# Performance work log

Hardware: AMD Instinct MI355X
Metric: run time of the kernel (lower is better)

## Reference

```python
import jax, jax.numpy as jnp
import numpy as np

B, IN, H, Z = 2048, 1024, 1024, 256


def setup_inputs() -> dict:
    key = jax.random.key(0)
    ks = jax.random.split(key, 17)
    s = 1.0 / np.sqrt(H)  # matches reset_parameters uniform(-stdv, stdv)
    u = lambda k, shape: jax.random.uniform(k, shape, minval=-s, maxval=s, dtype=jnp.float32)
    return {
        'src_x': jax.random.normal(ks[0], (B, IN), dtype=jnp.float32),
        'h': jax.random.normal(ks[1], (B, H), dtype=jnp.float32),
        'c': jax.random.normal(ks[2], (B, H), dtype=jnp.float32),
        'src_meta': jax.random.normal(ks[3], (B, Z), dtype=jnp.float32),
        'zh_w': u(ks[4], (4 * Z, Z)),
        'zh_b': u(ks[5], (4 * Z,)),
        'zx_w': u(ks[6], (4 * Z, Z)),
        'zx_b': u(ks[7], (4 * Z,)),
        'zb_w': u(ks[8], (4 * Z, Z)),
        'dh_w': u(ks[9], (4, H, Z)),
        'dx_w': u(ks[10], (4, H, Z)),
        'db_w': u(ks[11], (4, H, Z)),
        'db_b': u(ks[12], (4, H)),
        'w_h': u(ks[13], (4, H, H)),
        'w_x': u(ks[14], (4, H, IN)),
        'ln_w': u(ks[15], (4, H)),
        'ln_b': u(ks[16], (4, H)),
    }


def reference(src_x, h, c, src_meta, zh_w, zh_b, zx_w, zx_b, zb_w,
              dh_w, dx_w, db_w, db_b, w_h, w_x, ln_w, ln_b):
    b = src_x.shape[0]
    # hypernetwork projections, reshaped to [B, 4 gates, Z]
    zh = (src_meta @ zh_w.T + zh_b).reshape(b, 4, -1)
    zx = (src_meta @ zx_w.T + zx_b).reshape(b, 4, -1)
    zb = (src_meta @ zb_w.T).reshape(b, 4, -1)
    # per-gate scaling vectors d_h, d_x and bias d_b: [B, 4, H]
    d_h = jnp.einsum('bgz,ghz->bgh', zh, dh_w)
    d_x = jnp.einsum('bgz,ghz->bgh', zx, dx_w)
    d_b = jnp.einsum('bgz,ghz->bgh', zb, db_w) + db_b[None]
    # main LSTM matmuls: [B, 4, H]
    wh = jnp.einsum('ghj,bj->bgh', w_h, h)
    wx = jnp.einsum('ghj,bj->bgh', w_x, src_x)
    y = d_h * wh + d_x * wx + d_b
    # per-gate LayerNorm over hidden dim (eps = 1e-5, torch default)
    mu = jnp.mean(y, axis=-1, keepdims=True)
    var = jnp.var(y, axis=-1, keepdims=True)
    yn = (y - mu) * jax.lax.rsqrt(var + 1e-5) * ln_w[None] + ln_b[None]
    i, f, g, o = yn[:, 0], yn[:, 1], yn[:, 2], yn[:, 3]
    c_next = jax.nn.sigmoid(f) * c + jax.nn.sigmoid(i) * jnp.tanh(g)
    h_next = jax.nn.sigmoid(o) * jnp.tanh(c_next)
    return (h_next, c_next)
```

## Files before the change

### kernel.cpp

```cpp
#include <hip/hip_runtime.h>

typedef __attribute__((ext_vector_type(4))) float f32x4;
typedef __attribute__((ext_vector_type(16))) float f32x16;
typedef __attribute__((ext_vector_type(8))) short bf16x8;

#define DEVFN static __device__ __forceinline__

DEVFN unsigned short f2bf(float f) {
  union { float f; unsigned u; } x; x.f = f;
  unsigned r = x.u + 0x7fffu + ((x.u >> 16) & 1u);
  return (unsigned short)(r >> 16);
}
DEVFN float bf2f(unsigned short u) {
  union { unsigned u; float f; } x; x.u = ((unsigned)u) << 16;
  return x.f;
}

DEVFN void gload_lds16(const unsigned short* g, unsigned short* l) {
  __builtin_amdgcn_global_load_lds(
      (const __attribute__((address_space(1))) unsigned int*)g,
      (__attribute__((address_space(3))) unsigned int*)l, 16, 0, 0);
}

#define NSEG 8
struct SegTable {
  const float* src[NSEG];
  unsigned short* dst[NSEG];
  int chunks[NSEG];
};

__global__ __launch_bounds__(256) void prep_kernel(
    SegTable st, int castChunks,
    const float* __restrict__ zh_w, const float* __restrict__ zx_w,
    const float* __restrict__ zb_w, unsigned short* __restrict__ WzT,
    const float* __restrict__ zh_b, const float* __restrict__ zx_b,
    const float* __restrict__ db_b, const float* __restrict__ dh_w,
    const float* __restrict__ dx_w, float* __restrict__ F) {
  __shared__ float T[64][65];
  const int tid = threadIdx.x;
  int b = blockIdx.x;

  if (b < castChunks) {
    int c = b, s = 0;
    while (c >= st.chunks[s]) { c -= st.chunks[s]; ++s; }
    const float* src = st.src[s] + (long)c * 4096;
    unsigned short* dst = st.dst[s] + (long)c * 4096;
#pragma unroll
    for (int i = 0; i < 4; ++i) {
      float4 v = *(const float4*)(src + tid * 4 + i * 1024);
      ushort4 o;
      o.x = f2bf(v.x); o.y = f2bf(v.y); o.z = f2bf(v.z); o.w = f2bf(v.w);
      *(ushort4*)(dst + tid * 4 + i * 1024) = o;
    }
    return;
  }
  b -= castChunks;

  if (b < 192) {
    const int zz = b >> 4, rem = b & 15;
    const int t = zz >> 2, g = zz & 3;
    const float* src =
        (t == 0 ? zh_w : (t == 1 ? zx_w : zb_w)) + (long)g * 65536;
    unsigned short* dst = WzT + (long)zz * 65536;
    const int j0 = (rem & 3) * 64, k0 = (rem >> 2) * 64;
    const int jr = tid >> 2, kc = (tid & 3) * 16;
#pragma unroll
    for (int i = 0; i < 4; ++i) {
      float4 v = *(const float4*)(src + (long)(j0 + jr) * 256 + k0 + kc + i * 4);
      T[jr][kc + i * 4 + 0] = v.x;
      T[jr][kc + i * 4 + 1] = v.y;
      T[jr][kc + i * 4 + 2] = v.z;
      T[jr][kc + i * 4 + 3] = v.w;
    }
    __syncthreads();
    const int kr = tid >> 2, jc = (tid & 3) * 16;
    unsigned short tmp[16];
#pragma unroll
    for (int i = 0; i < 16; ++i) tmp[i] = f2bf(T[jc + i][kr]);
    *(bf16x8*)(dst + (long)(k0 + kr) * 256 + j0 + jc) = *(bf16x8*)&tmp[0];
    *(bf16x8*)(dst + (long)(k0 + kr) * 256 + j0 + jc + 8) = *(bf16x8*)&tmp[8];
    return;
  }
  b -= 192;

  if (b >= 128) {
    const int idx = (b - 128) * 1024 + tid * 4;
    *(float4*)(F + 8192 + idx) = *(const float4*)(db_b + idx);
    return;
  }
  const int wgid = b * 4 + (tid >> 6);
  const int lane = tid & 63;
  const int t = wgid >> 8, g = (wgid >> 6) & 3, hbase = (wgid & 63) * 16;
  const float* zb = (t == 0 ? zh_b : zx_b) + g * 256;
  const float* dw = (t == 0 ? dh_w : dx_w) + (long)g * 262144;
  float4 zv = *(const float4*)(zb + lane * 4);
#pragma unroll
  for (int i = 0; i < 16; ++i) {
    const int h = hbase + i;
    float4 wv = *(const float4*)(dw + (long)h * 256 + lane * 4);
    float s = zv.x * wv.x + zv.y * wv.y + zv.z * wv.z + zv.w * wv.w;
#pragma unroll
    for (int off = 32; off; off >>= 1) s += __shfl_down(s, off);
    if (lane == 0) F[(t * 4 + g) * 1024 + h] = s;
  }
}

DEVFN void gemm128_body(const unsigned short* __restrict__ A,
                        const unsigned short* __restrict__ W,
                        unsigned short* __restrict__ C,
                        const float* __restrict__ bias,
                        int lda, int ldb, int ldc, int K,
                        int bx, int by,
                        unsigned short* As, unsigned short* Bs) {
  const int m0 = by * 128, n0 = bx * 128;
  const int tid = threadIdx.x;
  const int lane = tid & 63, wid = tid >> 6;
  const int wr = wid >> 1, wc = wid & 1;

  const int srow = (tid >> 5) * 8 + (tid & 7);
  const int scol = ((tid >> 3) & 3) * 8;
  const unsigned short* Ag0 = A + (long)(m0 + srow) * lda + scol;
  const unsigned short* Ag1 = A + (long)(m0 + 64 + srow) * lda + scol;
  const unsigned short* Wg0 = W + (long)(n0 + srow) * ldb + scol;
  const unsigned short* Wg1 = W + (long)(n0 + 64 + srow) * ldb + scol;
  unsigned short* As0 = &As[tid * 8];
  unsigned short* As1 = &As[2048 + tid * 8];
  unsigned short* Bs0 = &Bs[tid * 8];
  unsigned short* Bs1 = &Bs[2048 + tid * 8];

  const int r = lane & 15, q = lane >> 4;

  f32x4 acc[4][4];
#pragma unroll
  for (int m = 0; m < 4; ++m)
#pragma unroll
    for (int n = 0; n < 4; ++n) acc[m][n] = (f32x4)0.f;

  for (int k0 = 0; k0 < K; k0 += 32) {
    gload_lds16(Ag0 + k0, As0);
    gload_lds16(Ag1 + k0, As1);
    gload_lds16(Wg0 + k0, Bs0);
    gload_lds16(Wg1 + k0, Bs1);
    __syncthreads();

    bf16x8 af[4], bfr[4];
#pragma unroll
    for (int m = 0; m < 4; ++m)
      af[m] = *(const bf16x8*)&As[(wr * 8 + m * 2 + (r >> 3)) * 256 +
                                  (r & 7) * 8 + q * 64];
#pragma unroll
    for (int n = 0; n < 4; ++n)
      bfr[n] = *(const bf16x8*)&Bs[(wc * 8 + n * 2 + (r >> 3)) * 256 +
                                   (r & 7) * 8 + q * 64];
#pragma unroll
    for (int m = 0; m < 4; ++m)
#pragma unroll
      for (int n = 0; n < 4; ++n)
        acc[m][n] = __builtin_amdgcn_mfma_f32_16x16x32_bf16(af[m], bfr[n],
                                                            acc[m][n], 0, 0, 0);
    __syncthreads();
  }

#pragma unroll
  for (int m = 0; m < 4; ++m) {
    const int row = m0 + wr * 64 + m * 16 + (lane >> 4) * 4;
#pragma unroll
    for (int n = 0; n < 4; ++n) {
      const int col = n0 + wc * 64 + n * 16 + r;
      float bv = bias ? bias[col] : 0.f;
#pragma unroll
      for (int j = 0; j < 4; ++j) {
        float v = acc[m][n][j] + bv;
        C[(long)(row + j) * ldc + col] = f2bf(v);
      }
    }
  }
}

__global__ __launch_bounds__(256) void gemm_e(
    const unsigned short* __restrict__ Wd, const unsigned short* __restrict__ WzT,
    unsigned short* __restrict__ E) {
  __shared__ __align__(16) unsigned short As[4096];
  __shared__ __align__(16) unsigned short Bs[4096];
  const int zz = blockIdx.z;
  gemm128_body(Wd + (long)zz * 262144, WzT + (long)zz * 65536,
               E + (long)zz * 262144, nullptr,
               256, 256, 256, 256, blockIdx.x, blockIdx.y, As, Bs);
}

__global__ __launch_bounds__(256) void gemm_d(
    const unsigned short* __restrict__ meta_bf, const unsigned short* __restrict__ E,
    unsigned short* __restrict__ dall, const float* __restrict__ F) {
  __shared__ __align__(16) unsigned short As[4096];
  __shared__ __align__(16) unsigned short Bs[4096];
  const int zz = blockIdx.z;
  unsigned short* C = dall + (long)(zz >> 2) * 8388608 + (zz & 3) * 1024;
  gemm128_body(meta_bf, E + (long)zz * 262144, C, F + zz * 1024,
               256, 256, 4096, 256, blockIdx.x, blockIdx.y, As, Bs);
}

__global__ __launch_bounds__(512, 2) void gemm256_whx(
    const unsigned short* __restrict__ Aall,
    const unsigned short* __restrict__ Ball,
    unsigned short* __restrict__ Call) {
  __shared__ __align__(16) unsigned short As[2][2][8192];
  __shared__ __align__(16) unsigned short Bs[2][2][8192];

  const int bid = blockIdx.x;
  const int swz = (bid & 7) * 32 + (bid >> 3);
  const int z = swz >> 7;
  const int rr = swz & 127;
  const int sb = rr >> 5, wq = rr & 31;
  const int my = (sb & 1) * 4 + (wq >> 3);
  const int nx = (sb >> 1) * 8 + (wq & 7);

  const unsigned short* Ag = Aall + (long)z * 2097152 + (long)my * 262144;
  const unsigned short* Bg = Ball + (long)z * 4194304 + (long)nx * 262144;
  unsigned short* Cg = Call + (long)z * 8388608 + (long)my * 1048576 + nx * 256;

  const int tid = threadIdx.x;
  const int lane = tid & 63, wid = tid >> 6;
  const int wm = wid >> 2, wn = wid & 3;
  const int l31 = lane & 31, l5 = lane >> 5;

  const int srow = (tid >> 6) * 8 + (tid & 7);
  const int gcol = ((tid >> 3) & 7) * 8;
  const unsigned short* AgS = Ag + (long)srow * 1024 + gcol;
  const unsigned short* BgS = Bg + (long)srow * 1024 + gcol;

  auto stageA = [&](int buf, int half, int kt) {
    const unsigned short* s = AgS + half * 131072 + kt * 64;
    unsigned short* d = &As[buf][half][tid * 8];
    gload_lds16(s, d);
    gload_lds16(s + 65536, d + 4096);
  };
  auto stageB = [&](int buf, int half, int kt) {
    const unsigned short* s = BgS + half * 131072 + kt * 64;
    unsigned short* d = &Bs[buf][half][tid * 8];
    gload_lds16(s, d);
    gload_lds16(s + 65536, d + 4096);
  };

  int koff[4];
#pragma unroll
  for (int ks = 0; ks < 4; ++ks) koff[ks] = (ks * 2 + l5) * 64;

  const int bhalf = wn >> 1;
  int brow[2];
#pragma unroll
  for (int nt = 0; nt < 2; ++nt)
    brow[nt] = ((wn & 1) * 8 + nt * 4 + (l31 >> 3)) * 512 + (l31 & 7) * 8;
  int arow[4];
#pragma unroll
  for (int mt = 0; mt < 4; ++mt)
    arow[mt] = (mt * 4 + (l31 >> 3)) * 512 + (l31 & 7) * 8;

  f32x16 acc[4][2];
#pragma unroll
  for (int m = 0; m < 4; ++m)
#pragma unroll
    for (int n = 0; n < 2; ++n) acc[m][n] = (f32x16)0.f;

  stageA(0, 0, 0); stageB(0, 0, 0); stageA(0, 1, 0); stageB(0, 1, 0);
  stageA(1, 0, 1); stageB(1, 0, 1);
  asm volatile("s_waitcnt vmcnt(4)" ::: "memory");
  __builtin_amdgcn_s_barrier();

#pragma unroll 2
  for (int T = 0; T < 16; ++T) {
    const int buf = T & 1, nb = buf ^ 1;

    if (T < 15) { stageA(nb, 1, T + 1); stageB(nb, 1, T + 1); }

    bf16x8 bfg[2][4], af[2][4];
    const unsigned short* Ab = &As[buf][wm][0];
    {
      const unsigned short* Bb = &Bs[buf][bhalf][0];
#pragma unroll
      for (int nt = 0; nt < 2; ++nt)
#pragma unroll
        for (int ks = 0; ks < 4; ++ks)
          bfg[nt][ks] = *(const bf16x8*)(Bb + brow[nt] + koff[ks]);
#pragma unroll
      for (int m2 = 0; m2 < 2; ++m2)
#pragma unroll
        for (int ks = 0; ks < 4; ++ks)
          af[m2][ks] = *(const bf16x8*)(Ab + arow[m2] + koff[ks]);
    }

    __builtin_amdgcn_s_setprio(1);
#pragma unroll
    for (int m2 = 0; m2 < 2; ++m2)
#pragma unroll
      for (int nt = 0; nt < 2; ++nt)
#pragma unroll
        for (int ks = 0; ks < 4; ++ks)
          acc[m2][nt] = __builtin_amdgcn_mfma_f32_32x32x16_bf16(
              af[m2][ks], bfg[nt][ks], acc[m2][nt], 0, 0, 0);
    __builtin_amdgcn_s_setprio(0);

#pragma unroll
    for (int m2 = 0; m2 < 2; ++m2)
#pragma unroll
      for (int ks = 0; ks < 4; ++ks)
        af[m2][ks] = *(const bf16x8*)(Ab + arow[2 + m2] + koff[ks]);

    asm volatile("s_waitcnt lgkmcnt(0)" ::: "memory");
    __builtin_amdgcn_sched_barrier(0);
    __builtin_amdgcn_s_barrier();

    if (T < 14) { stageA(buf, 0, T + 2); stageB(buf, 0, T + 2); }

    __builtin_amdgcn_s_setprio(1);
#pragma unroll
    for (int m2 = 0; m2 < 2; ++m2)
#pragma unroll
      for (int nt = 0; nt < 2; ++nt)
#pragma unroll
        for (int ks = 0; ks < 4; ++ks)
          acc[2 + m2][nt] = __builtin_amdgcn_mfma_f32_32x32x16_bf16(
              af[m2][ks], bfg[nt][ks], acc[2 + m2][nt], 0, 0, 0);
    __builtin_amdgcn_s_setprio(0);

    if (T < 14) {
      asm volatile("s_waitcnt vmcnt(4)" ::: "memory");
      __builtin_amdgcn_s_barrier();
    } else if (T == 14) {
      asm volatile("s_waitcnt vmcnt(0)" ::: "memory");
      __builtin_amdgcn_s_barrier();
    }
  }

#pragma unroll
  for (int mt = 0; mt < 4; ++mt) {
#pragma unroll
    for (int nt = 0; nt < 2; ++nt) {
      const int rb = wm * 128 + mt * 32 + 4 * l5;
      const int cb = wn * 64 + nt * 32 + l31;
#pragma unroll
      for (int reg = 0; reg < 16; ++reg) {
        const int row = rb + (reg & 3) + 8 * (reg >> 2);
        Cg[(long)row * 4096 + cb] = f2bf(acc[mt][nt][reg]);
      }
    }
  }
}

DEVFN void ld4bf(const unsigned short* p, float* o) {
  ushort4 v = *(const ushort4*)p;
  o[0] = bf2f(v.x); o[1] = bf2f(v.y); o[2] = bf2f(v.z); o[3] = bf2f(v.w);
}

__global__ __launch_bounds__(256) void epilogue_kernel(
    const unsigned short* __restrict__ d_all,
    const unsigned short* __restrict__ whx,
    const float* __restrict__ c_in,
    const float* __restrict__ ln_w, const float* __restrict__ ln_b,
    float* __restrict__ out) {
  const long b = blockIdx.x;
  const int t = threadIdx.x;
  const int lane = t & 63, wid = t >> 6;

  const unsigned short* dh = d_all + b * 4096;
  const unsigned short* dx = d_all + 8388608L + b * 4096;
  const unsigned short* db = d_all + 16777216L + b * 4096;
  const unsigned short* wh = whx + b * 4096;
  const unsigned short* wx = whx + 8388608L + b * 4096;

  __shared__ float redS[4][4], redQ[4][4];
  float y[4][4];

#pragma unroll
  for (int g = 0; g < 4; ++g) {
    const int base = g * 1024 + t * 4;
    float fdh[4], fdx[4], fdb[4], fwh[4], fwx[4];
    ld4bf(dh + base, fdh);
    ld4bf(dx + base, fdx);
    ld4bf(db + base, fdb);
    ld4bf(wh + base, fwh);
    ld4bf(wx + base, fwx);
    float s = 0.f, sq = 0.f;
#pragma unroll
    for (int j = 0; j < 4; ++j) {
      float v = fdh[j] * fwh[j] + fdx[j] * fwx[j] + fdb[j];
      y[g][j] = v;
      s += v;
      sq += v * v;
    }
#pragma unroll
    for (int off = 32; off; off >>= 1) {
      s += __shfl_down(s, off);
      sq += __shfl_down(sq, off);
    }
    if (lane == 0) { redS[g][wid] = s; redQ[g][wid] = sq; }
  }
  __syncthreads();

  float yn[4][4];
#pragma unroll
  for (int g = 0; g < 4; ++g) {
    float S = redS[g][0] + redS[g][1] + redS[g][2] + redS[g][3];
    float SQ = redQ[g][0] + redQ[g][1] + redQ[g][2] + redQ[g][3];
    float mu = S * (1.f / 1024.f);
    float var = SQ * (1.f / 1024.f) - mu * mu;
    float rs = rsqrtf(var + 1e-5f);
    const int base = g * 1024 + t * 4;
    float4 lw = *(const float4*)(ln_w + base);
    float4 lb = *(const float4*)(ln_b + base);
    yn[g][0] = (y[g][0] - mu) * rs * lw.x + lb.x;
    yn[g][1] = (y[g][1] - mu) * rs * lw.y + lb.y;
    yn[g][2] = (y[g][2] - mu) * rs * lw.z + lb.z;
    yn[g][3] = (y[g][3] - mu) * rs * lw.w + lb.w;
  }

  float4 cp = *(const float4*)(c_in + b * 1024 + t * 4);
  float cin[4] = {cp.x, cp.y, cp.z, cp.w};
  float hn[4], cn[4];
#pragma unroll
  for (int j = 0; j < 4; ++j) {
    float ii = yn[0][j], ff = yn[1][j], gg = yn[2][j], oo = yn[3][j];
    float si = 1.f / (1.f + expf(-ii));
    float sf = 1.f / (1.f + expf(-ff));
    float so = 1.f / (1.f + expf(-oo));
    float cnj = sf * cin[j] + si * tanhf(gg);
    cn[j] = cnj;
    hn[j] = so * tanhf(cnj);
  }
  float4 ho = {hn[0], hn[1], hn[2], hn[3]};
  float4 co = {cn[0], cn[1], cn[2], cn[3]};
  *(float4*)(out + b * 1024 + t * 4) = ho;
  *(float4*)(out + 2097152L + b * 1024 + t * 4) = co;
}

extern "C" void kernel_launch(void* const* d_in, const int* in_sizes, int n_in,
                              void* d_out, int out_size, void* d_ws,
                              size_t ws_size, hipStream_t stream) {
  const float* src_x = (const float*)d_in[0];
  const float* h_in  = (const float*)d_in[1];
  const float* c_in  = (const float*)d_in[2];
  const float* meta  = (const float*)d_in[3];
  const float* zh_w  = (const float*)d_in[4];
  const float* zh_b  = (const float*)d_in[5];
  const float* zx_w  = (const float*)d_in[6];
  const float* zx_b  = (const float*)d_in[7];
  const float* zb_w  = (const float*)d_in[8];
  const float* dh_w  = (const float*)d_in[9];
  const float* dx_w  = (const float*)d_in[10];
  const float* db_w  = (const float*)d_in[11];
  const float* db_b  = (const float*)d_in[12];
  const float* w_h   = (const float*)d_in[13];
  const float* w_x   = (const float*)d_in[14];
  const float* ln_w  = (const float*)d_in[15];
  const float* ln_b  = (const float*)d_in[16];

  char* ws = (char*)d_ws;
  unsigned short* h_bf    = (unsigned short*)(ws + 0);
  unsigned short* x_bf    = (unsigned short*)(ws + 4194304);
  unsigned short* meta_bf = (unsigned short*)(ws + 8388608);
  unsigned short* Wh      = (unsigned short*)(ws + 9437184);
  unsigned short* Wx      = (unsigned short*)(ws + 17825792);
  unsigned short* Wd      = (unsigned short*)(ws + 26214400);
  unsigned short* WzT     = (unsigned short*)(ws + 32505856);
  unsigned short* E       = (unsigned short*)(ws + 34078720);
  float*          F       = (float*)(ws + 40370176);
  unsigned short* dall    = (unsigned short*)(ws + 40419328);
  unsigned short* whx     = (unsigned short*)(ws + 90750976);
  if (ws_size < 124305408) return;

  SegTable st;
  int i = 0, total = 0;
  auto add = [&](const float* s, unsigned short* d, int n) {
    st.src[i] = s; st.dst[i] = d; st.chunks[i] = n / 4096;
    total += n / 4096; ++i;
  };
  add(h_in, h_bf, 2048 * 1024);
  add(src_x, x_bf, 2048 * 1024);
  add(meta, meta_bf, 2048 * 256);
  add(w_h, Wh, 4096 * 1024);
  add(w_x, Wx, 4096 * 1024);
  add(dh_w, Wd, 4 * 1024 * 256);
  add(dx_w, Wd + 1048576, 4 * 1024 * 256);
  add(db_w, Wd + 2097152, 4 * 1024 * 256);

  prep_kernel<<<total + 192 + 132, 256, 0, stream>>>(
      st, total, zh_w, zx_w, zb_w, WzT, zh_b, zx_b, db_b, dh_w, dx_w, F);

  gemm_e<<<dim3(2, 8, 12), 256, 0, stream>>>(Wd, WzT, E);

  gemm_d<<<dim3(8, 16, 12), 256, 0, stream>>>(meta_bf, E, dall, F);

  gemm256_whx<<<256, 512, 0, stream>>>(h_bf, Wh, whx);

  epilogue_kernel<<<2048, 256, 0, stream>>>(dall, whx, c_in, ln_w, ln_b,
                                            (float*)d_out);
}
```

Before: 137.4 us.

## Restructure main GEMM into four-phase 16x16 MFMA pipeline with XOR-swizzled LDS

```diff
diff --git a/kernel.cpp b/kernel.cpp
--- a/kernel.cpp
+++ b/kernel.cpp
@@ -1,7 +1,6 @@
 #include <hip/hip_runtime.h>
 
 typedef __attribute__((ext_vector_type(4))) float f32x4;
-typedef __attribute__((ext_vector_type(16))) float f32x16;
 typedef __attribute__((ext_vector_type(8))) short bf16x8;
 
 #define DEVFN static __device__ __forceinline__
@@ -117,8 +116,7 @@
   const int lane = tid & 63, wid = tid >> 6;
   const int wr = wid >> 1, wc = wid & 1;
 
-  const int srow = (tid >> 5) * 8 + (tid & 7);
-  const int scol = ((tid >> 3) & 3) * 8;
+  const int srow = tid >> 2, scol = (tid & 3) * 8;
   const unsigned short* Ag0 = A + (long)(m0 + srow) * lda + scol;
   const unsigned short* Ag1 = A + (long)(m0 + 64 + srow) * lda + scol;
   const unsigned short* Wg0 = W + (long)(n0 + srow) * ldb + scol;
@@ -146,12 +144,10 @@
     bf16x8 af[4], bfr[4];
 #pragma unroll
     for (int m = 0; m < 4; ++m)
-      af[m] = *(const bf16x8*)&As[(wr * 8 + m * 2 + (r >> 3)) * 256 +
-                                  (r & 7) * 8 + q * 64];
+      af[m] = *(const bf16x8*)&As[(wr * 64 + m * 16 + r) * 32 + q * 8];
 #pragma unroll
     for (int n = 0; n < 4; ++n)
-      bfr[n] = *(const bf16x8*)&Bs[(wc * 8 + n * 2 + (r >> 3)) * 256 +
-                                   (r & 7) * 8 + q * 64];
+      bfr[n] = *(const bf16x8*)&Bs[(wc * 64 + n * 16 + r) * 32 + q * 8];
 #pragma unroll
     for (int m = 0; m < 4; ++m)
 #pragma unroll
@@ -163,7 +159,7 @@
 
 #pragma unroll
   for (int m = 0; m < 4; ++m) {
-    const int row = m0 + wr * 64 + m * 16 + (lane >> 4) * 4;
+    const int row = m0 + wr * 64 + m * 16 + q * 4;
 #pragma unroll
     for (int n = 0; n < 4; ++n) {
       const int col = n0 + wc * 64 + n * 16 + r;
@@ -221,10 +217,11 @@
   const int tid = threadIdx.x;
   const int lane = tid & 63, wid = tid >> 6;
   const int wm = wid >> 2, wn = wid & 3;
-  const int l31 = lane & 31, l5 = lane >> 5;
-
-  const int srow = (tid >> 6) * 8 + (tid & 7);
-  const int gcol = ((tid >> 3) & 7) * 8;
+  const int fr = lane & 15, fq = lane >> 4;
+  const int s0 = fq ^ (fr & 7);
+
+  const int srow = tid >> 3, sslot = tid & 7;
+  const int gcol = (sslot ^ (srow & 7)) * 8;
   const unsigned short* AgS = Ag + (long)srow * 1024 + gcol;
   const unsigned short* BgS = Bg + (long)srow * 1024 + gcol;
 
@@ -241,109 +238,124 @@
     gload_lds16(s + 65536, d + 4096);
   };
 
-  int koff[4];
-#pragma unroll
-  for (int ks = 0; ks < 4; ++ks) koff[ks] = (ks * 2 + l5) * 64;
-
-  const int bhalf = wn >> 1;
-  int brow[2];
-#pragma unroll
-  for (int nt = 0; nt < 2; ++nt)
-    brow[nt] = ((wn & 1) * 8 + nt * 4 + (l31 >> 3)) * 512 + (l31 & 7) * 8;
-  int arow[4];
-#pragma unroll
-  for (int mt = 0; mt < 4; ++mt)
-    arow[mt] = (mt * 4 + (l31 >> 3)) * 512 + (l31 & 7) * 8;
-
-  f32x16 acc[4][2];
-#pragma unroll
-  for (int m = 0; m < 4; ++m)
-#pragma unroll
-    for (int n = 0; n < 2; ++n) acc[m][n] = (f32x16)0.f;
-
-  stageA(0, 0, 0); stageB(0, 0, 0); stageA(0, 1, 0); stageB(0, 1, 0);
-  stageA(1, 0, 1); stageB(1, 0, 1);
-  asm volatile("s_waitcnt vmcnt(4)" ::: "memory");
+  int aoff[4], boff[2];
+#pragma unroll
+  for (int mf = 0; mf < 4; ++mf)
+    aoff[mf] = (wm * 64 + mf * 16 + fr) * 64 + s0 * 8;
+#pragma unroll
+  for (int nf = 0; nf < 2; ++nf)
+    boff[nf] = (wn * 32 + nf * 16 + fr) * 64 + s0 * 8;
+
+  f32x4 acc[2][2][4][2];
+#pragma unroll
+  for (int i = 0; i < 2; ++i)
+#pragma unroll
+    for (int j = 0; j < 2; ++j)
+#pragma unroll
+      for (int m = 0; m < 4; ++m)
+#pragma unroll
+        for (int n = 0; n < 2; ++n) acc[i][j][m][n] = (f32x4)0.f;
+
+  stageA(0, 0, 0); stageA(0, 1, 0); stageB(0, 0, 0); stageB(0, 1, 0);
+  stageA(1, 0, 1); stageB(1, 0, 1); stageB(1, 1, 1);
+  asm volatile("s_waitcnt vmcnt(6)" ::: "memory");
   __builtin_amdgcn_s_barrier();
+
+  bf16x8 af[4][2], bA[2][2], bB[2][2];
+
+#define PH_SYNC                                          \
+  __builtin_amdgcn_s_barrier();                          \
+  asm volatile("s_waitcnt lgkmcnt(0)" ::: "memory");     \
+  __builtin_amdgcn_sched_barrier(0);
+
+#define PH_MFMA(MH, NH, BR)                              \
+  __builtin_amdgcn_s_setprio(1);                         \
+  _Pragma("unroll")                                      \
+  for (int mf = 0; mf < 4; ++mf)                         \
+    _Pragma("unroll")                                    \
+    for (int nf = 0; nf < 2; ++nf) {                     \
+      acc[MH][NH][mf][nf] = __builtin_amdgcn_mfma_f32_16x16x32_bf16( \
+          af[mf][0], BR[nf][0], acc[MH][NH][mf][nf], 0, 0, 0);       \
+      acc[MH][NH][mf][nf] = __builtin_amdgcn_mfma_f32_16x16x32_bf16( \
+          af[mf][1], BR[nf][1], acc[MH][NH][mf][nf], 0, 0, 0);       \
+    }                                                    \
+  __builtin_amdgcn_s_setprio(0);
 
 #pragma unroll 2
   for (int T = 0; T < 16; ++T) {
     const int buf = T & 1, nb = buf ^ 1;
 
-    if (T < 15) { stageA(nb, 1, T + 1); stageB(nb, 1, T + 1); }
-
-    bf16x8 bfg[2][4], af[2][4];
-    const unsigned short* Ab = &As[buf][wm][0];
     {
-      const unsigned short* Bb = &Bs[buf][bhalf][0];
-#pragma unroll
-      for (int nt = 0; nt < 2; ++nt)
-#pragma unroll
-        for (int ks = 0; ks < 4; ++ks)
-          bfg[nt][ks] = *(const bf16x8*)(Bb + brow[nt] + koff[ks]);
-#pragma unroll
-      for (int m2 = 0; m2 < 2; ++m2)
-#pragma unroll
-        for (int ks = 0; ks < 4; ++ks)
-          af[m2][ks] = *(const bf16x8*)(Ab + arow[m2] + koff[ks]);
-    }
-
-    __builtin_amdgcn_s_setprio(1);
-#pragma unroll
-    for (int m2 = 0; m2 < 2; ++m2)
-#pragma unroll
-      for (int nt = 0; nt < 2; ++nt)
-#pragma unroll
-        for (int ks = 0; ks < 4; ++ks)
-          acc[m2][nt] = __builtin_amdgcn_mfma_f32_32x32x16_bf16(
-              af[m2][ks], bfg[nt][ks], acc[m2][nt], 0, 0, 0);
-    __builtin_amdgcn_s_setprio(0);
-
-#pragma unroll
-    for (int m2 = 0; m2 < 2; ++m2)
-#pragma unroll
-      for (int ks = 0; ks < 4; ++ks)
-        af[m2][ks] = *(const bf16x8*)(Ab + arow[2 + m2] + koff[ks]);
-
-    asm volatile("s_waitcnt lgkmcnt(0)" ::: "memory");
-    __builtin_amdgcn_sched_barrier(0);
-    __builtin_amdgcn_s_barrier();
-
-    if (T < 14) { stageA(buf, 0, T + 2); stageB(buf, 0, T + 2); }
-
-    __builtin_amdgcn_s_setprio(1);
-#pragma unroll
-    for (int m2 = 0; m2 < 2; ++m2)
-#pragma unroll
-      for (int nt = 0; nt < 2; ++nt)
-#pragma unroll
-        for (int ks = 0; ks < 4; ++ks)
-          acc[2 + m2][nt] = __builtin_amdgcn_mfma_f32_32x32x16_bf16(
-              af[m2][ks], bfg[nt][ks], acc[2 + m2][nt], 0, 0, 0);
-    __builtin_amdgcn_s_setprio(0);
-
-    if (T < 14) {
-      asm volatile("s_waitcnt vmcnt(4)" ::: "memory");
+      const unsigned short* Ab = &As[buf][0][0];
+      const unsigned short* Bb = &Bs[buf][0][0];
+#pragma unroll
+      for (int mf = 0; mf < 4; ++mf) {
+        af[mf][0] = *(const bf16x8*)(Ab + aoff[mf]);
+        af[mf][1] = *(const bf16x8*)(Ab + (aoff[mf] ^ 32));
+      }
+#pragma unroll
+      for (int nf = 0; nf < 2; ++nf) {
+        bA[nf][0] = *(const bf16x8*)(Bb + boff[nf]);
+        bA[nf][1] = *(const bf16x8*)(Bb + (boff[nf] ^ 32));
+      }
+      if (T < 15) stageA(nb, 1, T + 1);
+      PH_SYNC;
+      PH_MFMA(0, 0, bA);
       __builtin_amdgcn_s_barrier();
-    } else if (T == 14) {
-      asm volatile("s_waitcnt vmcnt(0)" ::: "memory");
+    }
+    {
+      const unsigned short* Bb = &Bs[buf][1][0];
+#pragma unroll
+      for (int nf = 0; nf < 2; ++nf) {
+        bB[nf][0] = *(const bf16x8*)(Bb + boff[nf]);
+        bB[nf][1] = *(const bf16x8*)(Bb + (boff[nf] ^ 32));
+      }
+      if (T < 14) stageA(buf, 0, T + 2);
+      PH_SYNC;
+      PH_MFMA(0, 1, bB);
       __builtin_amdgcn_s_barrier();
     }
-  }
-
-#pragma unroll
-  for (int mt = 0; mt < 4; ++mt) {
-#pragma unroll
-    for (int nt = 0; nt < 2; ++nt) {
-      const int rb = wm * 128 + mt * 32 + 4 * l5;
-      const int cb = wn * 64 + nt * 32 + l31;
-#pragma unroll
-      for (int reg = 0; reg < 16; ++reg) {
-        const int row = rb + (reg & 3) + 8 * (reg >> 2);
-        Cg[(long)row * 4096 + cb] = f2bf(acc[mt][nt][reg]);
+    {
+      const unsigned short* Ab = &As[buf][1][0];
+#pragma unroll
+      for (int mf = 0; mf < 4; ++mf) {
+        af[mf][0] = *(const bf16x8*)(Ab + aoff[mf]);
+        af[mf][1] = *(const bf16x8*)(Ab + (aoff[mf] ^ 32));
       }
-    }
-  }
+      if (T < 14) stageB(buf, 0, T + 2);
+      PH_SYNC;
+      PH_MFMA(1, 0, bA);
+      __builtin_amdgcn_s_barrier();
+    }
+    {
+      if (T < 14) stageB(buf, 1, T + 2);
+      PH_SYNC;
+      PH_MFMA(1, 1, bB);
+      if (T < 14) {
+        asm volatile("s_waitcnt vmcnt(6)" ::: "memory");
+      } else if (T == 14) {
+        asm volatile("s_waitcnt vmcnt(0)" ::: "memory");
+      }
+      __builtin_amdgcn_s_barrier();
+    }
+  }
+#undef PH_SYNC
+#undef PH_MFMA
+
+#pragma unroll
+  for (int mh = 0; mh < 2; ++mh)
+#pragma unroll
+    for (int nh = 0; nh < 2; ++nh)
+#pragma unroll
+      for (int mf = 0; mf < 4; ++mf)
+#pragma unroll
+        for (int nf = 0; nf < 2; ++nf) {
+          const int row = mh * 128 + wm * 64 + mf * 16 + fq * 4;
+          const int col = nh * 128 + wn * 32 + nf * 16 + fr;
+#pragma unroll
+          for (int j = 0; j < 4; ++j)
+            Cg[(long)(row + j) * 4096 + col] = f2bf(acc[mh][nh][mf][nf][j]);
+        }
 }
 
 DEVFN void ld4bf(const unsigned short* p, float* o) {
```

After: 114.8 us. -16.5%, faster.
